# Performance work log

Hardware: AMD Instinct MI355X
Metric: run time of the kernel (lower is better)

The kernel has to match this reference:

```python
import jax, jax.numpy as jnp
import numpy as np

N = 100000      # nodes
E = 3200000     # edges (avg degree 32)
F_IN = 512      # input node features
H1, C1 = 8, 8   # layer-1: 8 heads x 8 channels -> concat 64
C2 = 7          # layer-2: 1 head, 7 classes
NEG_SLOPE = 0.2


def setup_inputs() -> dict:
    key = jax.random.key(0)
    ks = jax.random.split(key, 10)
    x = jax.random.normal(ks[0], (N, F_IN), jnp.float32)
    edge_index = jax.random.randint(ks[1], (2, E), 0, N, jnp.int32)
    s = 0.05
    return {
        "x": x,
        "edge_index": edge_index,
        "W1": jax.random.normal(ks[2], (F_IN, H1 * C1), jnp.float32) * s,
        "a_src1": jax.random.normal(ks[3], (H1, C1), jnp.float32) * s,
        "a_dst1": jax.random.normal(ks[4], (H1, C1), jnp.float32) * s,
        "b1": jnp.zeros((H1 * C1,), jnp.float32),
        "W2": jax.random.normal(ks[5], (H1 * C1, C2), jnp.float32) * s,
        "a_src2": jax.random.normal(ks[6], (1, C2), jnp.float32) * s,
        "a_dst2": jax.random.normal(ks[7], (1, C2), jnp.float32) * s,
        "b2": jnp.zeros((C2,), jnp.float32),
    }


def gat_conv(x, edge_index, W, a_src, a_dst, b, heads, out_ch):
    """PyG-style GATConv (concat=True, add_self_loops=True), eval mode (no dropout)."""
    n = x.shape[0]
    loops = jnp.arange(n, dtype=edge_index.dtype)
    src = jnp.concatenate([edge_index[0], loops])  # [E+N]
    dst = jnp.concatenate([edge_index[1], loops])
    h = (x @ W).reshape(n, heads, out_ch)           # [N,H,C]
    alpha_s = jnp.sum(h * a_src, axis=-1)           # [N,H]
    alpha_d = jnp.sum(h * a_dst, axis=-1)           # [N,H]
    e = jax.nn.leaky_relu(alpha_s[src] + alpha_d[dst], NEG_SLOPE)  # [E+N,H]
    # segment softmax over destination node
    m = jax.ops.segment_max(e, dst, num_segments=n)
    m = jnp.where(jnp.isfinite(m), m, 0.0)
    ex = jnp.exp(e - m[dst])
    denom = jax.ops.segment_sum(ex, dst, num_segments=n)
    alpha = ex / (denom[dst] + 1e-16)               # [E+N,H]
    out = jax.ops.segment_sum(h[src] * alpha[:, :, None], dst, num_segments=n)  # [N,H,C]
    return out.reshape(n, heads * out_ch) + b


def reference(x, edge_index, W1, a_src1, a_dst1, b1, W2, a_src2, a_dst2, b2):
    h = gat_conv(x, edge_index, W1, a_src1, a_dst1, b1, H1, C1)   # [N,64]
    h = gat_conv(h, edge_index, W2, a_src2, a_dst2, b2, 1, C2)    # [N,7]
    return jax.nn.log_softmax(h, axis=1)
```

## Files before the change

kernel.cpp:

```cpp
#include <hip/hip_runtime.h>
#include <hip/hip_bf16.h>

#define N_NODES 100000
#define N_EDGES 3200000
#define F_IN 512
#define NHEAD 8
#define CH1 8
#define F1 64
#define C2 7
#define NEG 0.2f
#define NBUCK 391

typedef __bf16 bf16x8 __attribute__((ext_vector_type(8)));
typedef float  f32x4  __attribute__((ext_vector_type(4)));
typedef unsigned int u32x4 __attribute__((ext_vector_type(4)));

union U4BF8 { u32x4 u; bf16x8 v; };

__device__ __forceinline__ float ldmix(const void* p, size_t i, int f32mode) {
  if (f32mode) return ((const float*)p)[i];
  union { unsigned short u; __bf16 b; } c;
  c.u = ((const unsigned short*)p)[i];
  return (float)c.b;
}

__global__ void detect_kernel(const unsigned int* __restrict__ x, int* __restrict__ flag) {
  int lane = threadIdx.x & 63;
  unsigned int w = x[lane];
  union { unsigned short u; __bf16 b; } c;
  c.u = (unsigned short)(w & 0xFFFFu);
  float v = (float)c.b;
  bool big = !(fabsf(v) <= 1e6f);
  unsigned long long m = __ballot(big);
  if (lane == 0) *flag = (m != 0ull) ? 1 : 0;
}

__global__ __launch_bounds__(256) void w1pack_kernel(
    const void* __restrict__ W1, __bf16* __restrict__ W1P, const int* __restrict__ flag)
{
  const int mode = *flag;
  int i = blockIdx.x * 256 + threadIdx.x;
  int wl = i >> 10; int t = (i >> 6) & 15; int lane = i & 63;
  int m = lane & 15, q = lane >> 4;
  int c0 = wl * 16;
  bf16x8 tv;
#pragma unroll
  for (int j = 0; j < 8; ++j)
    tv[j] = (__bf16)ldmix(W1, (size_t)(32*t + q*8 + j)*F1 + c0 + m, mode);
  *(bf16x8*)(W1P + (size_t)i * 8) = tv;
}

#define G1_ROWS 64
#define G1_CHUNK 256

__device__ __forceinline__ int g1_swz16(int g, int row) {
  return (g & 8) | ((g ^ row) & 7);
}

__device__ __forceinline__ void g1_stage(const char* xb, char* ldsbuf, int rowBase,
                                         int cByte, int wl, int lane, int rowBytes)
{
#pragma unroll
  for (int i = 0; i < 4; ++i) {
    int G   = ((i * 4 + wl) << 6) + lane;
    int row = G >> 4;
    int gp  = G & 15;
    int g   = g1_swz16(gp, row);
    int grow = rowBase + row; if (grow > N_NODES - 1) grow = N_NODES - 1;
    const char* src = xb + (size_t)grow * rowBytes + cByte + g * 16;
    __builtin_amdgcn_global_load_lds(
        (const __attribute__((address_space(1))) void*)src,
        (__attribute__((address_space(3))) void*)(ldsbuf + ((i * 4 + wl) << 10)),
        16, 0, 0);
  }
}

__device__ __forceinline__ void g1_comp_f32(const char* ldsbuf, const bf16x8* bfrag,
                                            f32x4* acc, int C, int m, int q)
{
#pragma unroll
  for (int rt = 0; rt < 4; ++rt) {
    const int row = rt * 16 + m;
    const char* rbase = ldsbuf + row * 256;
#pragma unroll
    for (int ks = 0; ks < 2; ++ks) {
      int g0 = ks * 8 + q * 2;
      int s0 = g1_swz16(g0, row);
      int s1 = g1_swz16(g0 + 1, row);
      f32x4 lo = *(const f32x4*)(rbase + s0 * 16);
      f32x4 hi = *(const f32x4*)(rbase + s1 * 16);
      bf16x8 av;
#pragma unroll
      for (int j = 0; j < 4; ++j) { av[j] = (__bf16)lo[j]; av[4 + j] = (__bf16)hi[j]; }
      acc[rt] = __builtin_amdgcn_mfma_f32_16x16x32_bf16(av, bfrag[C * 2 + ks], acc[rt], 0, 0, 0);
    }
  }
}

__device__ __forceinline__ void g1_comp_bf16(const char* ldsbuf, const bf16x8* bfrag,
                                             f32x4* acc, int C, int m, int q)
{
#pragma unroll
  for (int rt = 0; rt < 4; ++rt) {
    const int row = rt * 16 + m;
    const char* rbase = ldsbuf + row * 256;
#pragma unroll
    for (int ks = 0; ks < 4; ++ks) {
      int g0 = ks * 4 + q;
      int s0 = g1_swz16(g0, row);
      U4BF8 a;
      a.u = *(const u32x4*)(rbase + s0 * 16);
      acc[rt] = __builtin_amdgcn_mfma_f32_16x16x32_bf16(a.v, bfrag[C * 4 + ks], acc[rt], 0, 0, 0);
    }
  }
}

__global__ __launch_bounds__(256, 4) void gemm1_kernel(
    const void* __restrict__ x, const __bf16* __restrict__ W1P,
    __bf16* __restrict__ h1, const int* __restrict__ flag)
{
  __shared__ __align__(128) char lds[2][16384];
  const int mode = *flag;
  const int lane = threadIdx.x & 63;
  const int wl   = threadIdx.x >> 6;
  const int c0   = wl * 16;
  const int m    = lane & 15;
  const int q    = lane >> 4;

  const int rowBase = blockIdx.x * G1_ROWS;
  const char* xb = (const char*)x;
  const int RB = mode ? 2048 : 1024;

  g1_stage(xb, lds[0], rowBase, 0,        wl, lane, RB);
  g1_stage(xb, lds[1], rowBase, G1_CHUNK, wl, lane, RB);

  bf16x8 bfrag[16];
  const __bf16* wp = W1P + ((size_t)(wl * 16) * 64 + lane) * 8;
#pragma unroll
  for (int t = 0; t < 16; ++t) {
    U4BF8 a; a.u = *(const u32x4*)(wp + (size_t)t * 512);
    bfrag[t] = a.v;
  }

  f32x4 acc[4];
#pragma unroll
  for (int rt = 0; rt < 4; ++rt) acc[rt] = (f32x4){0.f, 0.f, 0.f, 0.f};

  __syncthreads();
  if (mode) {
#pragma unroll
    for (int c = 0; c < 8; ++c) {
      g1_comp_f32(lds[c & 1], bfrag, acc, c, m, q);
      __syncthreads();
      if (c + 2 < 8) g1_stage(xb, lds[c & 1], rowBase, (c + 2) * G1_CHUNK, wl, lane, RB);
    }
  } else {
#pragma unroll
    for (int c = 0; c < 4; ++c) {
      g1_comp_bf16(lds[c & 1], bfrag, acc, c, m, q);
      __syncthreads();
      if (c + 2 < 4) g1_stage(xb, lds[c & 1], rowBase, (c + 2) * G1_CHUNK, wl, lane, RB);
    }
  }

#pragma unroll
  for (int rt = 0; rt < 4; ++rt) {
#pragma unroll
    for (int j = 0; j < 4; ++j) {
      int row = rowBase + rt * 16 + q * 4 + j;
      if (row < N_NODES) h1[(size_t)row * F1 + c0 + m] = (__bf16)acc[rt][j];
    }
  }
}

__global__ __launch_bounds__(256) void alpha1_kernel(
    const __bf16* __restrict__ h1,
    const void* __restrict__ a_src, const void* __restrict__ a_dst,
    float* __restrict__ as, float* __restrict__ ad, const int* __restrict__ flag)
{
  const int mode = *flag;
  int i = blockIdx.x * 256 + threadIdx.x;
  if (i >= N_NODES * NHEAD) return;
  int h = i & 7;
  const __bf16* hp = h1 + (size_t)(i >> 3) * F1 + h * CH1;
  U4BF8 a; a.u = *(const u32x4*)hp;
  float s = 0.f, d = 0.f;
#pragma unroll
  for (int c = 0; c < CH1; ++c) {
    float hv = (float)a.v[c];
    s += hv * ldmix(a_src, h*CH1 + c, mode);
    d += hv * ldmix(a_dst, h*CH1 + c, mode);
  }
  as[i] = s; ad[i] = d;
}

__global__ __launch_bounds__(256) void buckhist_kernel(
    const int* __restrict__ ei, int* __restrict__ bh)
{
  __shared__ int h[NBUCK];
  for (int i = threadIdx.x; i < NBUCK; i += 256) h[i] = 0;
  __syncthreads();
  int start = blockIdx.x * 4096;
  for (int i = threadIdx.x; i < 4096; i += 256) {
    int e = start + i;
    if (e < N_EDGES) atomicAdd(&h[ei[N_EDGES + e] >> 8], 1);
  }
  __syncthreads();
  for (int i = threadIdx.x; i < NBUCK; i += 256) {
    int c = h[i];
    if (c) atomicAdd(&bh[i], c);
  }
}

__global__ __launch_bounds__(512) void buckscan_kernel(
    const int* __restrict__ bh, int* __restrict__ bb, int* __restrict__ bcur)
{
  __shared__ int s[512];
  int t = threadIdx.x;
  int v = (t < NBUCK) ? bh[t] : 0;
  s[t] = v;
  __syncthreads();
#pragma unroll
  for (int o = 1; o < 512; o <<= 1) {
    int u = (t >= o) ? s[t - o] : 0;
    __syncthreads();
    s[t] += u;
    __syncthreads();
  }
  if (t < NBUCK) { bb[t] = s[t] - v; bcur[t] = s[t] - v; }
  if (t == NBUCK - 1) bb[NBUCK] = s[t];
}

#define CHB 16384
__global__ __launch_bounds__(256) void buckscatter_kernel(
    const int* __restrict__ ei, int* __restrict__ bcur, int* __restrict__ pairs)
{
  __shared__ int h[NBUCK];
  __shared__ int base[NBUCK];
  for (int i = threadIdx.x; i < NBUCK; i += 256) h[i] = 0;
  __syncthreads();
  int start = blockIdx.x * CHB;
  for (int i = threadIdx.x; i < CHB; i += 256) {
    int e = start + i;
    if (e < N_EDGES) atomicAdd(&h[ei[N_EDGES + e] >> 8], 1);
  }
  __syncthreads();
  for (int i = threadIdx.x; i < NBUCK; i += 256) {
    int c = h[i];
    base[i] = c ? atomicAdd(&bcur[i], c) : 0;
    h[i] = 0;
  }
  __syncthreads();
  for (int i = threadIdx.x; i < CHB; i += 256) {
    int e = start + i;
    if (e < N_EDGES) {
      int dst = ei[N_EDGES + e];
      int src = ei[e];
      int b = dst >> 8;
      int pos = base[b] + atomicAdd(&h[b], 1);
      pairs[pos] = (src << 8) | (dst & 255);
    }
  }
}

__global__ __launch_bounds__(256) void csrbuild_kernel(
    const int* __restrict__ bb, const int* __restrict__ pairs,
    int* __restrict__ off, int* __restrict__ sorted)
{
  __shared__ int cnt[256];
  __shared__ int scan[256];
  int b = blockIdx.x;
  int lo = bb[b], hi = bb[b+1];
  int t = threadIdx.x;
  cnt[t] = 0;
  __syncthreads();
  for (int i = lo + t; i < hi; i += 256)
    atomicAdd(&cnt[pairs[i] & 255], 1);
  __syncthreads();
  int v = cnt[t];
  scan[t] = v;
  __syncthreads();
#pragma unroll
  for (int o = 1; o < 256; o <<= 1) {
    int u = (t >= o) ? scan[t - o] : 0;
    __syncthreads();
    scan[t] += u;
    __syncthreads();
  }
  int excl = scan[t] - v;
  int node = b * 256 + t;
  if (node < N_NODES) off[node] = lo + excl;
  if (b == 0 && t == 0) off[N_NODES] = N_EDGES;
  __syncthreads();
  cnt[t] = excl;
  __syncthreads();
  for (int i = lo + t; i < hi; i += 256) {
    int p = pairs[i];
    int w = lo + atomicAdd(&cnt[p & 255], 1);
    sorted[w] = p >> 8;
  }
}

__global__ __launch_bounds__(256) void aggregate1_kernel(
    const int* __restrict__ off, const int* __restrict__ sorted,
    const __bf16* __restrict__ h1,
    const float* __restrict__ as, const float* __restrict__ ad,
    const void* __restrict__ b1, __bf16* __restrict__ out1,
    const int* __restrict__ flag)
{
  __shared__ float wlds[4][64][8];
  const int mode = *flag;
  const int lane = threadIdx.x & 63;
  const int wl   = threadIdx.x >> 6;
  int n = blockIdx.x * 4 + wl;
  if (n >= N_NODES) return;
  const int h = lane >> 3;
  const float ad_h = ad[n*NHEAD + h];
  f32x4 adLo = *(const f32x4*)(ad + (size_t)n * 8);
  f32x4 adHi = *(const f32x4*)(ad + (size_t)n * 8 + 4);

  float e0 = as[n*NHEAD + h] + ad_h;
  e0 = e0 > 0.f ? e0 : NEG * e0;
  float w0 = __expf(e0);
  float acc = w0 * (float)h1[(size_t)n*F1 + lane];
  float den = w0;

  const int begin = off[n];
  const int cnt   = off[n+1] - begin;
  for (int base = 0; base < cnt; base += 64) {
    int idx = base + lane;
    bool vld = idx < cnt;
    int sv = vld ? sorted[begin + idx] : 0;
    f32x4 aLo = *(const f32x4*)(as + (size_t)sv * 8);
    f32x4 aHi = *(const f32x4*)(as + (size_t)sv * 8 + 4);
    f32x4 wLo, wHi;
#pragma unroll
    for (int k = 0; k < 4; ++k) {
      float e  = aLo[k] + adLo[k]; e  = e  > 0.f ? e  : NEG * e;
      float e2 = aHi[k] + adHi[k]; e2 = e2 > 0.f ? e2 : NEG * e2;
      wLo[k] = vld ? __expf(e)  : 0.f;
      wHi[k] = vld ? __expf(e2) : 0.f;
    }
    *(f32x4*)&wlds[wl][lane][0] = wLo;
    *(f32x4*)&wlds[wl][lane][4] = wHi;

    int jmax = cnt - base; if (jmax > 64) jmax = 64;
    for (int sub = 0; sub < jmax; sub += 16) {
#pragma unroll
      for (int jj = 0; jj < 16; ++jj) {
        int j = sub + jj;
        int src = __shfl(sv, j);
        float w = wlds[wl][j][h];
        float hv = (float)h1[(size_t)src*F1 + lane];
        acc += w * hv;
        den += w;
      }
    }
  }
  out1[(size_t)n*F1 + lane] = (__bf16)(acc / den + ldmix(b1, lane, mode));
}

__global__ __launch_bounds__(256) void h2_kernel(
    const __bf16* __restrict__ out1, const void* __restrict__ W2,
    const void* __restrict__ a_src2, const void* __restrict__ a_dst2,
    float* __restrict__ h2p, float* __restrict__ as2, float* __restrict__ ad2,
    const int* __restrict__ flag)
{
  const int mode = *flag;
  __shared__ float W2f[F1*C2];
  __shared__ float asw[C2], adw[C2];
  int t = threadIdx.x;
  for (int i = t; i < F1*C2; i += 256) W2f[i] = ldmix(W2, i, mode);
  if (t < C2) { asw[t] = ldmix(a_src2, t, mode); adw[t] = ldmix(a_dst2, t, mode); }
  __syncthreads();
  int n = blockIdx.x * 256 + t;
  if (n >= N_NODES) return;
  float r[F1];
  const u32x4* rp = (const u32x4*)(out1 + (size_t)n * F1);
#pragma unroll
  for (int k = 0; k < 8; ++k) {
    U4BF8 tv; tv.u = rp[k];
#pragma unroll
    for (int j = 0; j < 8; ++j) r[k*8 + j] = (float)tv.v[j];
  }
  float s = 0.f, d = 0.f;
#pragma unroll
  for (int c = 0; c < C2; ++c) {
    float acc = 0.f;
#pragma unroll
    for (int j = 0; j < F1; ++j) acc += r[j] * W2f[j*C2 + c];
    h2p[(size_t)n*8 + c] = acc;
    s += acc * asw[c]; d += acc * adw[c];
  }
  h2p[(size_t)n*8 + 7] = 0.f;
  as2[n] = s; ad2[n] = d;
}

__global__ __launch_bounds__(256) void aggregate2_kernel(
    const int* __restrict__ off, const int* __restrict__ sorted,
    const float* __restrict__ h2p,
    const float* __restrict__ as2, const float* __restrict__ ad2,
    const void* __restrict__ b2, void* __restrict__ outp,
    const int* __restrict__ flag)
{
  const int mode = *flag;
  const int lane = threadIdx.x & 63;
  const int c    = lane & 7;
  long long wid  = (long long)blockIdx.x * 4 + (threadIdx.x >> 6);
  int n = (int)(wid * 8 + (lane >> 3));
  bool valid = (n < N_NODES);
  if (!valid) n = N_NODES - 1;
  const float ad_n = ad2[n];

  float e0 = as2[n] + ad_n;
  e0 = e0 > 0.f ? e0 : NEG * e0;
  float w0 = __expf(e0);
  float acc = w0 * h2p[(size_t)n*8 + c];
  float den = w0;

  const int begin = off[n];
  const int cnt   = off[n+1] - begin;
  for (int base = 0; base < cnt; base += 8) {
    int idx = base + c;
    bool vld = idx < cnt;
    int sv = vld ? sorted[begin + idx] : 0;
    float e = as2[sv] + ad_n;
    e = e > 0.f ? e : NEG * e;
    float wo = vld ? __expf(e) : 0.f;
#pragma unroll
    for (int j = 0; j < 8; ++j) {
      int src  = __shfl(sv, j, 8);
      float w  = __shfl(wo, j, 8);
      float hv = h2p[(size_t)src*8 + c];
      acc += w * hv;
      den += w;
    }
  }

  float vv = acc / den + ldmix(b2, (c < 7) ? c : 0, mode);
  float mv = (c < 7) ? vv : -1e30f;
#pragma unroll
  for (int o = 1; o < 8; o <<= 1) mv = fmaxf(mv, __shfl_xor(mv, o, 8));
  float ex = (c < 7) ? __expf(vv - mv) : 0.f;
  float sum = ex;
#pragma unroll
  for (int o = 1; o < 8; o <<= 1) sum += __shfl_xor(sum, o, 8);
  float res = vv - (mv + __logf(sum));
  if (valid && c < 7) {
    if (mode) ((float*)outp)[(size_t)n*C2 + c] = res;
    else      ((__hip_bfloat16*)outp)[(size_t)n*C2 + c] = __float2bfloat16(res);
  }
}

extern "C" void kernel_launch(void* const* d_in, const int* in_sizes, int n_in,
                              void* d_out, int out_size, void* d_ws, size_t ws_size,
                              hipStream_t stream)
{
  const void* x    = d_in[0];
  const int*  ei   = (const int*)d_in[1];
  const void* W1   = d_in[2];
  const void* as1w = d_in[3];
  const void* ad1w = d_in[4];
  const void* b1   = d_in[5];
  const void* W2   = d_in[6];
  const void* as2w = d_in[7];
  const void* ad2w = d_in[8];
  const void* b2   = d_in[9];

  int*   flag = (int*)d_ws;
  float* ws   = (float*)d_ws + 16;

  float*  A      = ws;
  __bf16* h1b    = (__bf16*)A;
  float*  h2p    = A;
  float*  as2    = A + 800000;
  float*  ad2    = A + 900000;

  float*  as1    = ws + 3200000;
  float*  ad1    = ws + 4000000;
  __bf16* out1   = (__bf16*)(ws + 4800000);
  int*    pairs  = (int*)(ws + 4800000);
  int*    off    = (int*)(ws + 8000000);
  int*    bh     = (int*)(ws + 8110000);
  int*    bb     = (int*)(ws + 8112000);
  int*    bcur   = (int*)(ws + 8114000);
  __bf16* W1P    = (__bf16*)(ws + 8120000);
  int*    sorted = (int*)(ws + 8250000);

  detect_kernel<<<1, 64, 0, stream>>>((const unsigned int*)x, flag);
  w1pack_kernel<<<16, 256, 0, stream>>>(W1, W1P, flag);
  hipMemsetAsync(bh, 0, NBUCK * sizeof(int), stream);

  gemm1_kernel<<<(N_NODES + G1_ROWS - 1) / G1_ROWS, 256, 0, stream>>>(x, W1P, h1b, flag);
  alpha1_kernel<<<(N_NODES * NHEAD + 255) / 256, 256, 0, stream>>>(h1b, as1w, ad1w, as1, ad1, flag);

  buckhist_kernel<<<(N_EDGES + 4095) / 4096, 256, 0, stream>>>(ei, bh);
  buckscan_kernel<<<1, 512, 0, stream>>>(bh, bb, bcur);
  buckscatter_kernel<<<(N_EDGES + CHB - 1) / CHB, 256, 0, stream>>>(ei, bcur, pairs);
  csrbuild_kernel<<<NBUCK, 256, 0, stream>>>(bb, pairs, off, sorted);

  aggregate1_kernel<<<(N_NODES + 3) / 4, 256, 0, stream>>>(
      off, sorted, h1b, as1, ad1, b1, out1, flag);

  h2_kernel<<<(N_NODES + 255) / 256, 256, 0, stream>>>(out1, W2, as2w, ad2w, h2p, as2, ad2, flag);

  aggregate2_kernel<<<(N_NODES/8 + 3) / 4 + 1, 256, 0, stream>>>(
      off, sorted, h2p, as2, ad2, b2, d_out, flag);
}
```

Before: 622.9 us.

## Use finer CSR buckets and half-wave per node aggregation with packed bf16 loads

New measurement: 643.6 us. +3.3%, slower.

```diff
diff --git a/kernel.cpp b/kernel.cpp
--- a/kernel.cpp
+++ b/kernel.cpp
@@ -9,13 +9,21 @@
 #define F1 64
 #define C2 7
 #define NEG 0.2f
-#define NBUCK 391
+#define BSH 6
+#define BMSK 63
+#define NBUCK 1563
 
 typedef __bf16 bf16x8 __attribute__((ext_vector_type(8)));
 typedef float  f32x4  __attribute__((ext_vector_type(4)));
 typedef unsigned int u32x4 __attribute__((ext_vector_type(4)));
 
 union U4BF8 { u32x4 u; bf16x8 v; };
+
+__device__ __forceinline__ float bf2f(unsigned int bits16) {
+  union { unsigned int i; float f; } c;
+  c.i = bits16 << 16;
+  return c.f;
+}
 
 __device__ __forceinline__ float ldmix(const void* p, size_t i, int f32mode) {
   if (f32mode) return ((const float*)p)[i];
@@ -203,7 +211,7 @@
   int start = blockIdx.x * 4096;
   for (int i = threadIdx.x; i < 4096; i += 256) {
     int e = start + i;
-    if (e < N_EDGES) atomicAdd(&h[ei[N_EDGES + e] >> 8], 1);
+    if (e < N_EDGES) atomicAdd(&h[ei[N_EDGES + e] >> BSH], 1);
   }
   __syncthreads();
   for (int i = threadIdx.x; i < NBUCK; i += 256) {
@@ -212,26 +220,30 @@
   }
 }
 
-__global__ __launch_bounds__(512) void buckscan_kernel(
+__global__ __launch_bounds__(1024) void buckscan_kernel(
     const int* __restrict__ bh, int* __restrict__ bb, int* __restrict__ bcur)
 {
-  __shared__ int s[512];
+  __shared__ int s[1024];
   int t = threadIdx.x;
-  int v = (t < NBUCK) ? bh[t] : 0;
-  s[t] = v;
-  __syncthreads();
-#pragma unroll
-  for (int o = 1; o < 512; o <<= 1) {
+  int i0 = 2 * t, i1 = 2 * t + 1;
+  int v0 = (i0 < NBUCK) ? bh[i0] : 0;
+  int v1 = (i1 < NBUCK) ? bh[i1] : 0;
+  s[t] = v0 + v1;
+  __syncthreads();
+#pragma unroll
+  for (int o = 1; o < 1024; o <<= 1) {
     int u = (t >= o) ? s[t - o] : 0;
     __syncthreads();
     s[t] += u;
     __syncthreads();
   }
-  if (t < NBUCK) { bb[t] = s[t] - v; bcur[t] = s[t] - v; }
-  if (t == NBUCK - 1) bb[NBUCK] = s[t];
-}
-
-#define CHB 16384
+  int exclPair = s[t] - (v0 + v1);
+  if (i0 < NBUCK) { bb[i0] = exclPair;      bcur[i0] = exclPair; }
+  if (i1 < NBUCK) { bb[i1] = exclPair + v0; bcur[i1] = exclPair + v0; }
+  if (t == 1023) bb[NBUCK] = s[t];
+}
+
+#define CHB 4096
 __global__ __launch_bounds__(256) void buckscatter_kernel(
     const int* __restrict__ ei, int* __restrict__ bcur, int* __restrict__ pairs)
 {
@@ -242,7 +254,7 @@
   int start = blockIdx.x * CHB;
   for (int i = threadIdx.x; i < CHB; i += 256) {
     int e = start + i;
-    if (e < N_EDGES) atomicAdd(&h[ei[N_EDGES + e] >> 8], 1);
+    if (e < N_EDGES) atomicAdd(&h[ei[N_EDGES + e] >> BSH], 1);
   }
   __syncthreads();
   for (int i = threadIdx.x; i < NBUCK; i += 256) {
@@ -256,9 +268,9 @@
     if (e < N_EDGES) {
       int dst = ei[N_EDGES + e];
       int src = ei[e];
-      int b = dst >> 8;
+      int b = dst >> BSH;
       int pos = base[b] + atomicAdd(&h[b], 1);
-      pairs[pos] = (src << 8) | (dst & 255);
+      pairs[pos] = (src << BSH) | (dst & BMSK);
     }
   }
 }
@@ -267,37 +279,37 @@
     const int* __restrict__ bb, const int* __restrict__ pairs,
     int* __restrict__ off, int* __restrict__ sorted)
 {
-  __shared__ int cnt[256];
-  __shared__ int scan[256];
+  __shared__ int cnt[64];
+  __shared__ int scan[64];
   int b = blockIdx.x;
   int lo = bb[b], hi = bb[b+1];
   int t = threadIdx.x;
-  cnt[t] = 0;
+  if (t < 64) cnt[t] = 0;
   __syncthreads();
   for (int i = lo + t; i < hi; i += 256)
-    atomicAdd(&cnt[pairs[i] & 255], 1);
-  __syncthreads();
-  int v = cnt[t];
-  scan[t] = v;
-  __syncthreads();
-#pragma unroll
-  for (int o = 1; o < 256; o <<= 1) {
-    int u = (t >= o) ? scan[t - o] : 0;
+    atomicAdd(&cnt[pairs[i] & BMSK], 1);
+  __syncthreads();
+  if (t < 64) scan[t] = cnt[t];
+  __syncthreads();
+#pragma unroll
+  for (int o = 1; o < 64; o <<= 1) {
+    int u = (t < 64 && t >= o) ? scan[t - o] : 0;
     __syncthreads();
-    scan[t] += u;
+    if (t < 64) scan[t] += u;
     __syncthreads();
   }
-  int excl = scan[t] - v;
-  int node = b * 256 + t;
-  if (node < N_NODES) off[node] = lo + excl;
+  if (t < 64) {
+    int excl = scan[t] - cnt[t];
+    int node = b * 64 + t;
+    if (node < N_NODES) off[node] = lo + excl;
+    cnt[t] = excl;
+  }
   if (b == 0 && t == 0) off[N_NODES] = N_EDGES;
-  __syncthreads();
-  cnt[t] = excl;
   __syncthreads();
   for (int i = lo + t; i < hi; i += 256) {
     int p = pairs[i];
-    int w = lo + atomicAdd(&cnt[p & 255], 1);
-    sorted[w] = p >> 8;
+    int w = lo + atomicAdd(&cnt[p & BMSK], 1);
+    sorted[w] = p >> BSH;
   }
 }
 
@@ -308,27 +320,33 @@
     const void* __restrict__ b1, __bf16* __restrict__ out1,
     const int* __restrict__ flag)
 {
-  __shared__ float wlds[4][64][8];
+  __shared__ float wlds[4][2][32][8];
   const int mode = *flag;
   const int lane = threadIdx.x & 63;
   const int wl   = threadIdx.x >> 6;
-  int n = blockIdx.x * 4 + wl;
+  const int half = lane >> 5;
+  const int l32  = lane & 31;
+  const int h    = l32 >> 2;
+  const int col0 = l32 * 2;
+  int n = blockIdx.x * 8 + wl * 2 + half;
   if (n >= N_NODES) return;
-  const int h = lane >> 3;
-  const float ad_h = ad[n*NHEAD + h];
+
   f32x4 adLo = *(const f32x4*)(ad + (size_t)n * 8);
   f32x4 adHi = *(const f32x4*)(ad + (size_t)n * 8 + 4);
+  const float ad_h = ad[n*NHEAD + h];
 
   float e0 = as[n*NHEAD + h] + ad_h;
   e0 = e0 > 0.f ? e0 : NEG * e0;
   float w0 = __expf(e0);
-  float acc = w0 * (float)h1[(size_t)n*F1 + lane];
+  unsigned int sp = *(const unsigned int*)(h1 + (size_t)n*F1 + col0);
+  float acc0 = w0 * bf2f(sp & 0xffffu);
+  float acc1 = w0 * bf2f(sp >> 16);
   float den = w0;
 
   const int begin = off[n];
   const int cnt   = off[n+1] - begin;
-  for (int base = 0; base < cnt; base += 64) {
-    int idx = base + lane;
+  for (int base = 0; base < cnt; base += 32) {
+    int idx = base + l32;
     bool vld = idx < cnt;
     int sv = vld ? sorted[begin + idx] : 0;
     f32x4 aLo = *(const f32x4*)(as + (size_t)sv * 8);
@@ -341,23 +359,28 @@
       wLo[k] = vld ? __expf(e)  : 0.f;
       wHi[k] = vld ? __expf(e2) : 0.f;
     }
-    *(f32x4*)&wlds[wl][lane][0] = wLo;
-    *(f32x4*)&wlds[wl][lane][4] = wHi;
-
-    int jmax = cnt - base; if (jmax > 64) jmax = 64;
+    *(f32x4*)&wlds[wl][half][l32][0] = wLo;
+    *(f32x4*)&wlds[wl][half][l32][4] = wHi;
+
+    int jmax = cnt - base; if (jmax > 32) jmax = 32;
     for (int sub = 0; sub < jmax; sub += 16) {
 #pragma unroll
       for (int jj = 0; jj < 16; ++jj) {
         int j = sub + jj;
-        int src = __shfl(sv, j);
-        float w = wlds[wl][j][h];
-        float hv = (float)h1[(size_t)src*F1 + lane];
-        acc += w * hv;
-        den += w;
+        int src = __shfl(sv, j, 32);
+        float w = wlds[wl][half][j][h];
+        unsigned int hp = *(const unsigned int*)(h1 + (size_t)src*F1 + col0);
+        acc0 += w * bf2f(hp & 0xffffu);
+        acc1 += w * bf2f(hp >> 16);
+        den  += w;
       }
     }
   }
-  out1[(size_t)n*F1 + lane] = (__bf16)(acc / den + ldmix(b1, lane, mode));
+  float r0 = acc0 / den + ldmix(b1, col0,     mode);
+  float r1 = acc1 / den + ldmix(b1, col0 + 1, mode);
+  union { __bf16 b[2]; unsigned int u; } pk;
+  pk.b[0] = (__bf16)r0; pk.b[1] = (__bf16)r1;
+  *(unsigned int*)(out1 + (size_t)n*F1 + col0) = pk.u;
 }
 
 __global__ __launch_bounds__(256) void h2_kernel(
@@ -495,11 +518,11 @@
   alpha1_kernel<<<(N_NODES * NHEAD + 255) / 256, 256, 0, stream>>>(h1b, as1w, ad1w, as1, ad1, flag);
 
   buckhist_kernel<<<(N_EDGES + 4095) / 4096, 256, 0, stream>>>(ei, bh);
-  buckscan_kernel<<<1, 512, 0, stream>>>(bh, bb, bcur);
+  buckscan_kernel<<<1, 1024, 0, stream>>>(bh, bb, bcur);
   buckscatter_kernel<<<(N_EDGES + CHB - 1) / CHB, 256, 0, stream>>>(ei, bcur, pairs);
   csrbuild_kernel<<<NBUCK, 256, 0, stream>>>(bb, pairs, off, sorted);
 
-  aggregate1_kernel<<<(N_NODES + 3) / 4, 256, 0, stream>>>(
+  aggregate1_kernel<<<(N_NODES + 7) / 8, 256, 0, stream>>>(
       off, sorted, h1b, as1, ad1, b1, out1, flag);
 
   h2_kernel<<<(N_NODES + 255) / 256, 256, 0, stream>>>(out1, W2, as2w, ad2w, h2p, as2, ad2, flag);
```
